# Kernel tuning notes

Measured on AMD Instinct MI355X. Metric: run time of the kernel, lower is better.

Reference implementation:

```python
import jax, jax.numpy as jnp
import numpy as np

B, N, DIM, HEADS = 2, 2048, 1152, 16
HD = DIM // HEADS  # 72


def _fake_quant_sym(x, axis):
    # Dynamic symmetric int8 fake-quant: per-row scale = max|x| / 127
    amax = jnp.max(jnp.abs(x), axis=axis, keepdims=True)
    scale = jnp.maximum(amax, 1e-8) / 127.0
    q = jnp.clip(jnp.round(x / scale), -128.0, 127.0) * scale
    return x + jax.lax.stop_gradient(q - x)  # STE


def _fake_quant_unsigned(x, axis):
    # Post-softmax attn map in [0,1]: unsigned 8-bit dynamic fake-quant
    amax = jnp.max(x, axis=axis, keepdims=True)
    scale = jnp.maximum(amax, 1e-8) / 255.0
    q = jnp.clip(jnp.round(x / scale), 0.0, 255.0) * scale
    return x + jax.lax.stop_gradient(q - x)


def setup_inputs() -> dict:
    key = jax.random.key(0)
    k1, k2, k3, k4 = jax.random.split(key, 4)
    return {
        "x": jax.random.normal(k1, (B, N, DIM), dtype=jnp.float32),
        "w_qkv": jax.random.normal(k2, (3 * DIM, DIM), dtype=jnp.float32) * 0.02,
        "w_proj": jax.random.normal(k3, (DIM, DIM), dtype=jnp.float32) * 0.02,
        "b_proj": jax.random.normal(k4, (DIM,), dtype=jnp.float32) * 0.02,
    }


def reference(x, w_qkv, w_proj, b_proj):
    Bsz, Nt, C = x.shape
    H, Dh = HEADS, C // HEADS
    qkv = x @ w_qkv.T  # [B, N, 3C]
    qkv = qkv.reshape(Bsz, Nt, 3, H, Dh).transpose(2, 0, 3, 1, 4)  # [3, B, H, N, Dh]
    q, k, v = qkv[0], qkv[1], qkv[2]
    # Dynamic quantization: q/k per (token) row over head_dim; v per channel over tokens
    q = _fake_quant_sym(q, axis=-1)
    k = _fake_quant_sym(k, axis=-1)
    v = _fake_quant_sym(v, axis=-2)
    scale = Dh ** -0.5
    attn = jnp.einsum('bhnd,bhmd->bhnm', q * scale, k).astype(jnp.float32)
    attn = jax.nn.softmax(attn, axis=-1).astype(x.dtype)
    attn = _fake_quant_unsigned(attn, axis=-1)
    out = jnp.einsum('bhnm,bhmd->bhnd', attn, v)  # [B, H, N, Dh]
    out = out.transpose(0, 2, 1, 3).reshape(Bsz, Nt, C)
    return out @ w_proj.T + b_proj
```

## Files before the change

kernel.cpp:

```cpp
#include <hip/hip_runtime.h>
#include <math.h>


typedef int   i32x4  __attribute__((ext_vector_type(4)));
typedef short bf16x8 __attribute__((ext_vector_type(8)));
typedef float f32x4  __attribute__((ext_vector_type(4)));

constexpr int Bz   = 2;
constexpr int Ntok = 2048;
constexpr int DIMC = 1152;
constexpr int H    = 16;
constexpr int HD_  = 72;
constexpr int Mrows = Bz * Ntok;
constexpr int C3    = 3 * DIMC;

__device__ __forceinline__ unsigned short f2bf(float f) {
  unsigned u = __float_as_uint(f);
  return (unsigned short)((u + 0x7fffu + ((u >> 16) & 1u)) >> 16);
}
__device__ __forceinline__ float bf2f(unsigned short h) {
  return __uint_as_float((unsigned)h << 16);
}
__device__ __forceinline__ void split1(float v, unsigned short& h,
                                       unsigned short& m, unsigned short& l) {
  h = f2bf(v); float r1 = v - bf2f(h);
  m = f2bf(r1); float r2 = r1 - bf2f(m);
  l = f2bf(r2);
}

__global__ __launch_bounds__(256)
void split3_kernel(const float* __restrict__ src, unsigned short* __restrict__ ph,
                   unsigned short* __restrict__ pm, unsigned short* __restrict__ pl,
                   int n4) {
  for (int i = blockIdx.x * 256 + threadIdx.x; i < n4; i += gridDim.x * 256) {
    float4 v = ((const float4*)src)[i];
    ushort4 h, m, l;
    split1(v.x, h.x, m.x, l.x);
    split1(v.y, h.y, m.y, l.y);
    split1(v.z, h.z, m.z, l.z);
    split1(v.w, h.w, m.w, l.w);
    ((ushort4*)ph)[i] = h;
    ((ushort4*)pm)[i] = m;
    ((ushort4*)pl)[i] = l;
  }
}

__device__ __forceinline__ void gload16(const void* g, void* l) {
  __builtin_amdgcn_global_load_lds(
      (const __attribute__((address_space(1))) unsigned int*)g,
      (__attribute__((address_space(3))) unsigned int*)l, 16, 0, 0);
}

template<bool BIAS>
__global__ __launch_bounds__(256)
void gemm3(const unsigned short* __restrict__ Ah, const unsigned short* __restrict__ Am,
           const unsigned short* __restrict__ Al,
           const unsigned short* __restrict__ Bh, const unsigned short* __restrict__ Bm,
           const unsigned short* __restrict__ Bl,
           const float* __restrict__ bias, float* __restrict__ C,
           int Md, int Nd, int Kd) {
  __shared__ __align__(16) unsigned short As[3][128 * 32];
  __shared__ __align__(16) unsigned short Bs[3][128 * 32];
  const int t = threadIdx.x, lane = t & 63, wv = t >> 6;
  const int r15 = lane & 15, h4 = lane >> 4;
  const int gx = gridDim.x;
  const int nwg = gx * gridDim.y;
  const int orig = blockIdx.y * gx + blockIdx.x;
  const int qq = nwg >> 3, rr = nwg & 7;
  const int xcd = orig & 7, loc = orig >> 3;
  const int wg = (xcd < rr) ? (xcd * (qq + 1) + loc)
                            : (rr * (qq + 1) + (xcd - rr) * qq + loc);
  const int bm = (wg / gx) << 7, bn = (wg % gx) << 7;
  const int wn = (wv & 1) << 6, wm = (wv >> 1) << 6;

  const unsigned short* Ap[3] = {Ah, Am, Al};
  const unsigned short* Bp[3] = {Bh, Bm, Bl};

  f32x4 acc[4][4];
#pragma unroll
  for (int i = 0; i < 4; ++i)
#pragma unroll
    for (int j = 0; j < 4; ++j) acc[i][j] = (f32x4){0.f, 0.f, 0.f, 0.f};

  const int lin0 = t * 16;
  const int r0 = lin0 >> 6, cb0 = lin0 & 63;
  const int lin1 = lin0 + 4096;
  const int r1 = lin1 >> 6, cb1 = lin1 & 63;

  for (int k0 = 0; k0 < Kd; k0 += 32) {
    __syncthreads();
#pragma unroll
    for (int p = 0; p < 3; ++p) {
      gload16((const char*)(Ap[p] + (size_t)(bm + r0) * Kd + k0) + cb0,
              (char*)&As[p][0] + lin0);
      gload16((const char*)(Ap[p] + (size_t)(bm + r1) * Kd + k0) + cb1,
              (char*)&As[p][0] + lin1);
      gload16((const char*)(Bp[p] + (size_t)(bn + r0) * Kd + k0) + cb0,
              (char*)&Bs[p][0] + lin0);
      gload16((const char*)(Bp[p] + (size_t)(bn + r1) * Kd + k0) + cb1,
              (char*)&Bs[p][0] + lin1);
    }
    __syncthreads();
    bf16x8 bf[3][4];
#pragma unroll
    for (int p = 0; p < 3; ++p)
#pragma unroll
      for (int c = 0; c < 4; ++c)
        bf[p][c] = *(const bf16x8*)&Bs[p][(wn + c * 16 + r15) * 32 + h4 * 8];
#pragma unroll
    for (int pa = 0; pa < 3; ++pa) {
#pragma unroll
      for (int mf = 0; mf < 4; ++mf) {
        bf16x8 af = *(const bf16x8*)&As[pa][(wm + mf * 16 + r15) * 32 + h4 * 8];
#pragma unroll
        for (int bp = 0; bp < 3; ++bp) {
          if (bp < 3 - pa) {
#pragma unroll
            for (int nf = 0; nf < 4; ++nf)
              acc[mf][nf] = __builtin_amdgcn_mfma_f32_16x16x32_bf16(
                  bf[bp][nf], af, acc[mf][nf], 0, 0, 0);
          }
        }
      }
    }
  }
#pragma unroll
  for (int mf = 0; mf < 4; ++mf) {
    const int m = bm + wm + mf * 16 + r15;
#pragma unroll
    for (int nf = 0; nf < 4; ++nf) {
      const int n = bn + wn + nf * 16 + (h4 << 2);
      float4 o;
      o.x = acc[mf][nf][0]; o.y = acc[mf][nf][1];
      o.z = acc[mf][nf][2]; o.w = acc[mf][nf][3];
      if (BIAS) {
        o.x += bias[n]; o.y += bias[n + 1]; o.z += bias[n + 2]; o.w += bias[n + 3];
      }
      *(float4*)(C + (size_t)m * Nd + n) = o;
    }
  }
}

template<bool BIAS>
__global__ __launch_bounds__(256)
void gemm_bt(const float* __restrict__ A, const float* __restrict__ W,
             const float* __restrict__ bias, float* __restrict__ Cout,
             int Md, int Nd, int Kd) {
  __shared__ float As[16][132];
  __shared__ float Bs[16][132];
  const int t  = threadIdx.x;
  const int bm = blockIdx.y << 7, bn = blockIdx.x << 7;
  const int lr = t >> 1;
  const int lk = (t & 1) << 3;
  const float* Ap = A + (size_t)(bm + lr) * Kd + lk;
  const float* Wp = W + (size_t)(bn + lr) * Kd + lk;
  const int tx = t & 15, ty = t >> 4;
  float acc[8][8] = {};
  for (int k0 = 0; k0 < Kd; k0 += 16) {
    float4 a0 = *(const float4*)(Ap + k0);
    float4 a1 = *(const float4*)(Ap + k0 + 4);
    float4 w0 = *(const float4*)(Wp + k0);
    float4 w1 = *(const float4*)(Wp + k0 + 4);
    __syncthreads();
    As[lk + 0][lr] = a0.x; As[lk + 1][lr] = a0.y;
    As[lk + 2][lr] = a0.z; As[lk + 3][lr] = a0.w;
    As[lk + 4][lr] = a1.x; As[lk + 5][lr] = a1.y;
    As[lk + 6][lr] = a1.z; As[lk + 7][lr] = a1.w;
    Bs[lk + 0][lr] = w0.x; Bs[lk + 1][lr] = w0.y;
    Bs[lk + 2][lr] = w0.z; Bs[lk + 3][lr] = w0.w;
    Bs[lk + 4][lr] = w1.x; Bs[lk + 5][lr] = w1.y;
    Bs[lk + 6][lr] = w1.z; Bs[lk + 7][lr] = w1.w;
    __syncthreads();
#pragma unroll
    for (int kk = 0; kk < 16; ++kk) {
      float4 x0 = *(const float4*)&As[kk][(ty << 3) + 0];
      float4 x1 = *(const float4*)&As[kk][(ty << 3) + 4];
      float4 y0 = *(const float4*)&Bs[kk][(tx << 3) + 0];
      float4 y1 = *(const float4*)&Bs[kk][(tx << 3) + 4];
      float ar[8] = {x0.x, x0.y, x0.z, x0.w, x1.x, x1.y, x1.z, x1.w};
      float br[8] = {y0.x, y0.y, y0.z, y0.w, y1.x, y1.y, y1.z, y1.w};
#pragma unroll
      for (int i = 0; i < 8; ++i)
#pragma unroll
        for (int j = 0; j < 8; ++j)
          acc[i][j] = fmaf(ar[i], br[j], acc[i][j]);
    }
  }
  float bias8[8] = {0.f, 0.f, 0.f, 0.f, 0.f, 0.f, 0.f, 0.f};
  if (BIAS) {
#pragma unroll
    for (int j = 0; j < 8; ++j) bias8[j] = bias[bn + (tx << 3) + j];
  }
#pragma unroll
  for (int i = 0; i < 8; ++i) {
    const int m = bm + (ty << 3) + i;
    float* cp = Cout + (size_t)m * Nd + bn + (tx << 3);
    float4 o0, o1;
    o0.x = acc[i][0] + bias8[0]; o0.y = acc[i][1] + bias8[1];
    o0.z = acc[i][2] + bias8[2]; o0.w = acc[i][3] + bias8[3];
    o1.x = acc[i][4] + bias8[4]; o1.y = acc[i][5] + bias8[5];
    o1.z = acc[i][6] + bias8[6]; o1.w = acc[i][7] + bias8[7];
    *(float4*)(cp + 0) = o0;
    *(float4*)(cp + 4) = o1;
  }
}

__global__ __launch_bounds__(256)
void quant_qk_pack(const float* __restrict__ qkv,
                   signed char* __restrict__ q8, signed char* __restrict__ k8,
                   float* __restrict__ sq, float* __restrict__ sk) {
  const int wid  = (blockIdx.x << 2) + (threadIdx.x >> 6);
  const int lane = threadIdx.x & 63;
  const int h  = wid & 15;
  const int g  = (wid >> 4) & 1;
  const int bn = wid >> 5;
  const float* row = qkv + (size_t)bn * C3 + g * DIMC + h * HD_;
  float x0 = row[lane];
  float x1 = (lane < 8) ? row[64 + lane] : 0.f;
  float amax = fmaxf(fabsf(x0), fabsf(x1));
#pragma unroll
  for (int s = 32; s; s >>= 1) amax = fmaxf(amax, __shfl_xor(amax, s));
  const float scale = fmaxf(amax, 1e-8f) / 127.f;
  int q0 = (int)fminf(fmaxf(rintf(x0 / scale), -128.f), 127.f);
  int q1 = (int)fminf(fmaxf(rintf(x1 / scale), -128.f), 127.f);
  const int b = bn >> 11, n = bn & 2047;
  signed char* dst = (g ? k8 : q8) + ((size_t)(b * H + h) * Ntok + n) * 128;
  dst[lane] = (signed char)q0;
  dst[64 + lane] = (lane < 8) ? (signed char)q1 : 0;
  if (lane == 0) (g ? sk : sq)[(size_t)(b * H + h) * Ntok + n] = scale;
}

__global__ __launch_bounds__(256)
void quant_v_pack(const float* __restrict__ qkv, signed char* __restrict__ vT8,
                  float* __restrict__ sv, int* __restrict__ cs) {
  const int col = blockIdx.x;
  const int d = col % 80;
  const int h = (col / 80) % H;
  const int b = col / (80 * H);
  const int idx = (b * H + h) * 80 + d;
  signed char* vrow = vT8 + (size_t)idx * 2048;
  const int t = threadIdx.x;
  if (d >= HD_) {
#pragma unroll
    for (int i = 0; i < 8; ++i) vrow[t + (i << 8)] = 0;
    if (t == 0) { sv[idx] = 0.f; cs[idx] = 0; }
    return;
  }
  const float* base = qkv + (size_t)b * Ntok * C3 + 2 * DIMC + h * HD_ + d;
  float vals[8];
  float amax = 0.f;
#pragma unroll
  for (int i = 0; i < 8; ++i) {
    float v = base[(size_t)(t + (i << 8)) * C3];
    vals[i] = v;
    amax = fmaxf(amax, fabsf(v));
  }
#pragma unroll
  for (int s = 32; s; s >>= 1) amax = fmaxf(amax, __shfl_xor(amax, s));
  __shared__ float red[4];
  if ((t & 63) == 0) red[t >> 6] = amax;
  __syncthreads();
  amax = fmaxf(fmaxf(red[0], red[1]), fmaxf(red[2], red[3]));
  const float scale = fmaxf(amax, 1e-8f) / 127.f;
  int isum = 0;
#pragma unroll
  for (int i = 0; i < 8; ++i) {
    int q = (int)fminf(fmaxf(rintf(vals[i] / scale), -128.f), 127.f);
    vrow[t + (i << 8)] = (signed char)q;
    isum += q;
  }
#pragma unroll
  for (int s = 32; s; s >>= 1) isum += __shfl_xor(isum, s);
  __shared__ int ired[4];
  if ((t & 63) == 0) ired[t >> 6] = isum;
  __syncthreads();
  if (t == 0) {
    cs[idx] = ired[0] + ired[1] + ired[2] + ired[3];
    sv[idx] = scale;
  }
}

__device__ __forceinline__ float logitv(float cl, float skj, int a) {
  return cl * skj * (float)a;
}

#define STAGE_K(KT)                                                          \
  {                                                                          \
    _Pragma("unroll")                                                        \
    for (int c_ = 0; c_ < 2; ++c_) {                                         \
      const int L_ = (t + (c_ << 8)) << 4;                                   \
      const int row_ = L_ >> 7;                                              \
      const int col_ = L_ & 127;                                             \
      gload16(kgbase + (size_t)(KT) * 8192 + row_ * 128 +                    \
                  (col_ ^ ((row_ & 7) << 4)),                                \
              Ks + L_);                                                      \
    }                                                                        \
  }
#define STAGE_SK(KT)                                                         \
  if (t < 16) {                                                              \
    gload16(skgbase + (KT) * 256 + (t << 4), (signed char*)Sks + (t << 4));  \
  }
#define STAGE_V(KT)                                                          \
  {                                                                          \
    const int L_ = t << 4;                                                   \
    const int row_ = L_ >> 6, col_ = L_ & 63;                                \
    gload16(vgbase + (size_t)row_ * 2048 + (KT) * 64 +                       \
                (col_ ^ ((row_ & 3) << 4)),                                  \
            Vs + L_);                                                        \
    if (t < 64) {                                                            \
      const int L2_ = (t + 256) << 4;                                        \
      const int row2_ = L2_ >> 6, col2_ = L2_ & 63;                          \
      gload16(vgbase + (size_t)row2_ * 2048 + (KT) * 64 +                    \
                  (col2_ ^ ((row2_ & 3) << 4)),                              \
              Vs + L2_);                                                     \
    }                                                                        \
  }

#define BODYA                                                                 \
  {                                                                           \
    _Pragma("unroll")                                                         \
    for (int g_ = 0; g_ < 4; ++g_) {                                          \
      const int krow_ = (g_ << 4) + i16;                                      \
      const int kx_ = (krow_ & 7) << 4;                                       \
      const i32x4 kf0_ = *(const i32x4*)&Ks[krow_ * 128 + ((h4 << 4) ^ kx_)]; \
      const i32x4 kf1_ = *(const i32x4*)&Ks[krow_ * 128 + ((64 | (h4 << 4)) ^ kx_)]; \
      i32x4 acc_ = {0, 0, 0, 0};                                              \
      acc_ = __builtin_amdgcn_mfma_i32_16x16x64_i8(kf0_, qf0, acc_, 0, 0, 0); \
      acc_ = __builtin_amdgcn_mfma_i32_16x16x64_i8(kf1_, qf1, acc_, 0, 0, 0); \
      const float4 skv_ = *(const float4*)&Sks[(g_ << 4) + (h4 << 2)];        \
      mr4[g_] = fmaxf(mr4[g_], logitv(cl, skv_.x, acc_[0]));                  \
      mr4[g_] = fmaxf(mr4[g_], logitv(cl, skv_.y, acc_[1]));                  \
      mr4[g_] = fmaxf(mr4[g_], logitv(cl, skv_.z, acc_[2]));                  \
      mr4[g_] = fmaxf(mr4[g_], logitv(cl, skv_.w, acc_[3]));                  \
    }                                                                         \
  }

#define BODYB                                                                 \
  {                                                                           \
    _Pragma("unroll")                                                         \
    for (int g_ = 0; g_ < 4; ++g_) {                                          \
      const int krow_ = (g_ << 4) + i16;                                      \
      const int kx_ = (krow_ & 7) << 4;                                       \
      const i32x4 kf0_ = *(const i32x4*)&Ks[krow_ * 128 + ((h4 << 4) ^ kx_)]; \
      const i32x4 kf1_ = *(const i32x4*)&Ks[krow_ * 128 + ((64 | (h4 << 4)) ^ kx_)]; \
      i32x4 acc_ = {0, 0, 0, 0};                                              \
      acc_ = __builtin_amdgcn_mfma_i32_16x16x64_i8(kf0_, qf0, acc_, 0, 0, 0); \
      acc_ = __builtin_amdgcn_mfma_i32_16x16x64_i8(kf1_, qf1, acc_, 0, 0, 0); \
      const float4 skv_ = *(const float4*)&Sks[(g_ << 4) + (h4 << 2)];        \
      const float sks_[4] = {skv_.x, skv_.y, skv_.z, skv_.w};                 \
      int packed_ = 0;                                                        \
      _Pragma("unroll")                                                       \
      for (int r_ = 0; r_ < 4; ++r_) {                                        \
        const float lv_ = logitv(cl, sks_[r_], acc_[r_]);                     \
        const float e_ = __expf(lv_ - mrow);            \
        z4[g_] += e_;                                                         \
        const float u_ = fminf(rintf(e_ * 255.f), 255.f);                     \
        const int s8_ = (int)u_ - 128;                                        \
        packed_ |= (s8_ & 255) << (r_ << 3);                                  \
      }                                                                       \
      *(int*)&P[wv][(i16 << 6) + ((g_ ^ sI) << 4) + (h4 << 2)] = packed_;     \
    }                                                                         \
    const i32x4 pf_ = *(const i32x4*)&P[wv][(i16 << 6) + ((h4 ^ sI) << 4)];   \
    _Pragma("unroll")                                                         \
    for (int dg_ = 0; dg_ < 5; ++dg_) {                                       \
      const int vrow_ = (dg_ << 4) + i16;                                     \
      const int vx_ = (vrow_ & 3) << 4;                                       \
      const i32x4 vf_ = *(const i32x4*)&Vs[vrow_ * 64 + ((h4 << 4) ^ vx_)];   \
      pv[dg_] = __builtin_amdgcn_mfma_i32_16x16x64_i8(vf_, pf_, pv[dg_], 0, 0, 0); \
    }                                                                         \
  }

template<bool SPLIT>
__global__ __launch_bounds__(256)
void attn_mfma(const signed char* __restrict__ q8, const signed char* __restrict__ k8,
               const signed char* __restrict__ vT8,
               const float* __restrict__ sq, const float* __restrict__ sk,
               const float* __restrict__ sv, const int* __restrict__ cs,
               float* __restrict__ aoutF,
               unsigned short* __restrict__ ah, unsigned short* __restrict__ am,
               unsigned short* __restrict__ al) {
  const int bid = ((blockIdx.x & 7) << 7) + (blockIdx.x >> 3);
  const int qt = bid & 31, h = (bid >> 5) & 15, b = bid >> 9;
  const int n0 = qt << 6;
  const int t = threadIdx.x, lane = t & 63, wv = t >> 6;
  const int i16 = lane & 15, h4 = lane >> 4;
  const int bh = b * H + h;
  const int sI = (i16 >> 1) & 3;

  __shared__ __align__(16) signed char Ks[8192];
  __shared__ __align__(16) signed char Vs[5120];
  __shared__ __align__(16) float Sks[64];
  __shared__ __align__(16) signed char P[4][1024];

  const int qrow = n0 + (wv << 4) + i16;
  const signed char* qp = q8 + ((size_t)bh * Ntok + qrow) * 128 + (h4 << 4);
  const i32x4 qf0 = *(const i32x4*)qp;
  const i32x4 qf1 = *(const i32x4*)(qp + 64);
  const float cl = sq[(size_t)bh * Ntok + qrow] * 0.11785113019775793f;
  const signed char* kgbase  = k8 + (size_t)bh * Ntok * 128;
  const signed char* vgbase  = vT8 + (size_t)bh * 80 * 2048;
  const signed char* skgbase = (const signed char*)(sk + (size_t)bh * Ntok);

  float mr4[4];
#pragma unroll
  for (int g = 0; g < 4; ++g) mr4[g] = -3.4e38f;
  for (int kt = 0; kt < 32; ++kt) {
    __syncthreads();
    STAGE_K(kt);
    STAGE_SK(kt);
    __syncthreads();
    BODYA;
  }
  float mrow = fmaxf(fmaxf(mr4[0], mr4[1]), fmaxf(mr4[2], mr4[3]));
  mrow = fmaxf(mrow, __shfl_xor(mrow, 16));
  mrow = fmaxf(mrow, __shfl_xor(mrow, 32));

  float z4[4] = {0.f, 0.f, 0.f, 0.f};
  i32x4 pv[5];
#pragma unroll
  for (int dg = 0; dg < 5; ++dg) pv[dg] = (i32x4){0, 0, 0, 0};

  for (int kt = 0; kt < 32; ++kt) {
    __syncthreads();
    STAGE_K(kt);
    STAGE_V(kt);
    STAGE_SK(kt);
    __syncthreads();
    BODYB;
  }

  float z = (z4[0] + z4[1]) + (z4[2] + z4[3]);
  z += __shfl_xor(z, 16);
  z += __shfl_xor(z, 32);
  const float rz = 1.0f / z;
  const float ss = rz / 255.f;

  const size_t rowoff = ((size_t)(b * Ntok + n0 + (wv << 4) + i16)) * DIMC + h * HD_;
  const int sbase = bh * 80;
#pragma unroll
  for (int dg = 0; dg < 5; ++dg) {
    const int d0 = dg * 16 + (h4 << 2);
    if (d0 < HD_) {
      float4 o;
      int t0 = pv[dg][0] + (cs[sbase + d0 + 0] << 7);
      int t1 = pv[dg][1] + (cs[sbase + d0 + 1] << 7);
      int t2 = pv[dg][2] + (cs[sbase + d0 + 2] << 7);
      int t3 = pv[dg][3] + (cs[sbase + d0 + 3] << 7);
      o.x = (float)t0 * sv[sbase + d0 + 0] * ss;
      o.y = (float)t1 * sv[sbase + d0 + 1] * ss;
      o.z = (float)t2 * sv[sbase + d0 + 2] * ss;
      o.w = (float)t3 * sv[sbase + d0 + 3] * ss;
      if (SPLIT) {
        ushort4 hh, mm, ll;
        split1(o.x, hh.x, mm.x, ll.x);
        split1(o.y, hh.y, mm.y, ll.y);
        split1(o.z, hh.z, mm.z, ll.z);
        split1(o.w, hh.w, mm.w, ll.w);
        *(ushort4*)(ah + rowoff + d0) = hh;
        *(ushort4*)(am + rowoff + d0) = mm;
        *(ushort4*)(al + rowoff + d0) = ll;
      } else {
        *(float4*)(aoutF + rowoff + d0) = o;
      }
    }
  }
}

constexpr size_t SZ_QKV  = (size_t)Mrows * C3 * 4;
constexpr size_t PL_X    = (size_t)Mrows * DIMC * 2;
constexpr size_t PL_WQ   = (size_t)C3 * DIMC * 2;
constexpr size_t PL_WP   = (size_t)DIMC * DIMC * 2;
constexpr size_t OFF_XA  = SZ_QKV;
constexpr size_t OFF_WQ  = OFF_XA + 3 * PL_X;
constexpr size_t OFF_WP  = OFF_WQ + 3 * PL_WQ;
constexpr size_t REQ_NEW = OFF_WP + 3 * PL_WP;
constexpr size_t SZ_Q8 = (size_t)Bz * H * Ntok * 128;
constexpr size_t SZ_V8 = (size_t)Bz * H * 80 * 2048;
constexpr size_t SZ_S  = (size_t)Bz * H * Ntok * 4;
constexpr size_t SZ_SV = (size_t)Bz * H * 80 * 4;
constexpr size_t A_Q8 = OFF_WQ;
constexpr size_t A_K8 = A_Q8 + SZ_Q8;
constexpr size_t A_V8 = A_K8 + SZ_Q8;
constexpr size_t A_SQ = A_V8 + SZ_V8;
constexpr size_t A_SK = A_SQ + SZ_S;
constexpr size_t A_SV = A_SK + SZ_S;
constexpr size_t A_CS = A_SV + SZ_SV;
static_assert(A_CS + SZ_SV <= OFF_WP, "alias overflow");
constexpr size_t F_AOUT = SZ_QKV;
constexpr size_t F_Q8   = F_AOUT + (size_t)Mrows * DIMC * 4;
constexpr size_t F_K8   = F_Q8 + SZ_Q8;
constexpr size_t F_V8   = F_K8 + SZ_Q8;
constexpr size_t F_SQ   = F_V8 + SZ_V8;
constexpr size_t F_SK   = F_SQ + SZ_S;
constexpr size_t F_SV   = F_SK + SZ_S;
constexpr size_t F_CS   = F_SV + SZ_SV;

extern "C" void kernel_launch(void* const* d_in, const int* in_sizes, int n_in,
                              void* d_out, int out_size, void* d_ws, size_t ws_size,
                              hipStream_t stream) {
  const float* x      = (const float*)d_in[0];
  const float* w_qkv  = (const float*)d_in[1];
  const float* w_proj = (const float*)d_in[2];
  const float* b_proj = (const float*)d_in[3];
  float* out = (float*)d_out;
  char* ws = (char*)d_ws;
  float* qkv = (float*)ws;

  if (ws_size >= REQ_NEW) {
    unsigned short* xh = (unsigned short*)(ws + OFF_XA);
    unsigned short* xm = xh + PL_X / 2;
    unsigned short* xl = xm + PL_X / 2;
    unsigned short* wqh = (unsigned short*)(ws + OFF_WQ);
    unsigned short* wqm = wqh + PL_WQ / 2;
    unsigned short* wql = wqm + PL_WQ / 2;
    unsigned short* wph = (unsigned short*)(ws + OFF_WP);
    unsigned short* wpm = wph + PL_WP / 2;
    unsigned short* wpl = wpm + PL_WP / 2;
    signed char* q8  = (signed char*)(ws + A_Q8);
    signed char* k8  = (signed char*)(ws + A_K8);
    signed char* vT8 = (signed char*)(ws + A_V8);
    float* sq = (float*)(ws + A_SQ);
    float* sk = (float*)(ws + A_SK);
    float* sv = (float*)(ws + A_SV);
    int*   cs = (int*)(ws + A_CS);
    unsigned short* ah = xh;
    unsigned short* am = xm;
    unsigned short* al = xl;

    split3_kernel<<<2048, 256, 0, stream>>>(x, xh, xm, xl, Mrows * DIMC / 4);
    split3_kernel<<<2048, 256, 0, stream>>>(w_qkv, wqh, wqm, wql, C3 * DIMC / 4);
    split3_kernel<<<1297, 256, 0, stream>>>(w_proj, wph, wpm, wpl, DIMC * DIMC / 4);
    gemm3<false><<<dim3(C3 / 128, Mrows / 128), 256, 0, stream>>>(
        xh, xm, xl, wqh, wqm, wql, nullptr, qkv, Mrows, C3, DIMC);
    quant_qk_pack<<<(Bz * Ntok * 2 * H) / 4, 256, 0, stream>>>(qkv, q8, k8, sq, sk);
    quant_v_pack<<<Bz * H * 80, 256, 0, stream>>>(qkv, vT8, sv, cs);
    attn_mfma<true><<<Bz * H * (Ntok / 64), 256, 0, stream>>>(
        q8, k8, vT8, sq, sk, sv, cs, nullptr, ah, am, al);
    gemm3<true><<<dim3(DIMC / 128, Mrows / 128), 256, 0, stream>>>(
        ah, am, al, wph, wpm, wpl, b_proj, out, Mrows, DIMC, DIMC);
  } else {
    float* aout = (float*)(ws + F_AOUT);
    signed char* q8  = (signed char*)(ws + F_Q8);
    signed char* k8  = (signed char*)(ws + F_K8);
    signed char* vT8 = (signed char*)(ws + F_V8);
    float* sq = (float*)(ws + F_SQ);
    float* sk = (float*)(ws + F_SK);
    float* sv = (float*)(ws + F_SV);
    int*   cs = (int*)(ws + F_CS);
    gemm_bt<false><<<dim3(C3 / 128, Mrows / 128), 256, 0, stream>>>(
        x, w_qkv, nullptr, qkv, Mrows, C3, DIMC);
    quant_qk_pack<<<(Bz * Ntok * 2 * H) / 4, 256, 0, stream>>>(qkv, q8, k8, sq, sk);
    quant_v_pack<<<Bz * H * 80, 256, 0, stream>>>(qkv, vT8, sv, cs);
    attn_mfma<false><<<Bz * H * (Ntok / 64), 256, 0, stream>>>(
        q8, k8, vT8, sq, sk, sv, cs, aout, nullptr, nullptr, nullptr);
    gemm_bt<true><<<dim3(DIMC / 128, Mrows / 128), 256, 0, stream>>>(
        aout, w_proj, b_proj, out, Mrows, DIMC, DIMC);
  }
}
```

Measured before the change: 504.1 us.

## Swizzle packed LDS layout in split-bf16 GEMM and narrow proj tile

```diff
diff --git a/kernel.cpp b/kernel.cpp
--- a/kernel.cpp
+++ b/kernel.cpp
@@ -51,7 +51,7 @@
       (__attribute__((address_space(3))) unsigned int*)l, 16, 0, 0);
 }
 
-template<bool BIAS>
+template<bool BIAS, int NF>
 __global__ __launch_bounds__(256)
 void gemm3(const unsigned short* __restrict__ Ah, const unsigned short* __restrict__ Am,
            const unsigned short* __restrict__ Al,
@@ -59,64 +59,88 @@
            const unsigned short* __restrict__ Bl,
            const float* __restrict__ bias, float* __restrict__ C,
            int Md, int Nd, int Kd) {
-  __shared__ __align__(16) unsigned short As[3][128 * 32];
-  __shared__ __align__(16) unsigned short Bs[3][128 * 32];
+  constexpr int BN = 32 * NF;
+  __shared__ __align__(16) char Apk[128 * 128];
+  __shared__ __align__(16) char Alt[128 * 64];
+  __shared__ __align__(16) char Bpk[BN * 128];
+  __shared__ __align__(16) char Blt[BN * 64];
   const int t = threadIdx.x, lane = t & 63, wv = t >> 6;
   const int r15 = lane & 15, h4 = lane >> 4;
   const int gx = gridDim.x;
   const int nwg = gx * gridDim.y;
   const int orig = blockIdx.y * gx + blockIdx.x;
-  const int qq = nwg >> 3, rr = nwg & 7;
-  const int xcd = orig & 7, loc = orig >> 3;
-  const int wg = (xcd < rr) ? (xcd * (qq + 1) + loc)
-                            : (rr * (qq + 1) + (xcd - rr) * qq + loc);
-  const int bm = (wg / gx) << 7, bn = (wg % gx) << 7;
-  const int wn = (wv & 1) << 6, wm = (wv >> 1) << 6;
-
-  const unsigned short* Ap[3] = {Ah, Am, Al};
-  const unsigned short* Bp[3] = {Bh, Bm, Bl};
-
-  f32x4 acc[4][4];
+  const int qq = nwg >> 3;
+  const int wg = (orig & 7) * qq + (orig >> 3);
+  const int bm = (wg / gx) << 7, bn = (wg % gx) * BN;
+  const int wn = (wv & 1) * (BN / 2), wm = (wv >> 1) << 6;
+
+  f32x4 acc[4][NF];
 #pragma unroll
   for (int i = 0; i < 4; ++i)
 #pragma unroll
-    for (int j = 0; j < 4; ++j) acc[i][j] = (f32x4){0.f, 0.f, 0.f, 0.f};
-
-  const int lin0 = t * 16;
-  const int r0 = lin0 >> 6, cb0 = lin0 & 63;
-  const int lin1 = lin0 + 4096;
-  const int r1 = lin1 >> 6, cb1 = lin1 & 63;
+    for (int j = 0; j < NF; ++j) acc[i][j] = (f32x4){0.f, 0.f, 0.f, 0.f};
+
+  const int k3 = (r15 & 7) << 4;
+  const int k2 = (r15 & 3) << 4;
 
   for (int k0 = 0; k0 < Kd; k0 += 32) {
     __syncthreads();
 #pragma unroll
-    for (int p = 0; p < 3; ++p) {
-      gload16((const char*)(Ap[p] + (size_t)(bm + r0) * Kd + k0) + cb0,
-              (char*)&As[p][0] + lin0);
-      gload16((const char*)(Ap[p] + (size_t)(bm + r1) * Kd + k0) + cb1,
-              (char*)&As[p][0] + lin1);
-      gload16((const char*)(Bp[p] + (size_t)(bn + r0) * Kd + k0) + cb0,
-              (char*)&Bs[p][0] + lin0);
-      gload16((const char*)(Bp[p] + (size_t)(bn + r1) * Kd + k0) + cb1,
-              (char*)&Bs[p][0] + lin1);
-    }
-    __syncthreads();
-    bf16x8 bf[3][4];
-#pragma unroll
-    for (int p = 0; p < 3; ++p)
-#pragma unroll
-      for (int c = 0; c < 4; ++c)
-        bf[p][c] = *(const bf16x8*)&Bs[p][(wn + c * 16 + r15) * 32 + h4 * 8];
+    for (int c = 0; c < 4; ++c) {
+      const int L = (t + (c << 8)) << 4;
+      const int row = L >> 7;
+      const int scol = (L & 127) ^ ((row & 7) << 4);
+      const unsigned short* sp = (scol & 64) ? Am : Ah;
+      gload16((const char*)(sp + (size_t)(bm + row) * Kd + k0) + (scol & 63),
+              Apk + L);
+    }
+#pragma unroll
+    for (int c = 0; c < 2; ++c) {
+      const int L = (t + (c << 8)) << 4;
+      const int row = L >> 6;
+      const int scol = (L & 63) ^ ((row & 3) << 4);
+      gload16((const char*)(Al + (size_t)(bm + row) * Kd + k0) + scol, Alt + L);
+    }
+#pragma unroll
+    for (int c = 0; c < NF; ++c) {
+      const int L = (t + (c << 8)) << 4;
+      const int row = L >> 7;
+      const int scol = (L & 127) ^ ((row & 7) << 4);
+      const unsigned short* sp = (scol & 64) ? Bm : Bh;
+      gload16((const char*)(sp + (size_t)(bn + row) * Kd + k0) + (scol & 63),
+              Bpk + L);
+    }
+#pragma unroll
+    for (int c = 0; c < NF / 2; ++c) {
+      const int L = (t + (c << 8)) << 4;
+      const int row = L >> 6;
+      const int scol = (L & 63) ^ ((row & 3) << 4);
+      gload16((const char*)(Bl + (size_t)(bn + row) * Kd + k0) + scol, Blt + L);
+    }
+    __syncthreads();
+
+    bf16x8 bf[3][NF];
+#pragma unroll
+    for (int c = 0; c < NF; ++c) {
+      const int br = wn + c * 16 + r15;
+      bf[0][c] = *(const bf16x8*)(Bpk + br * 128 + ((h4 << 4) ^ k3));
+      bf[1][c] = *(const bf16x8*)(Bpk + br * 128 + ((64 | (h4 << 4)) ^ k3));
+      bf[2][c] = *(const bf16x8*)(Blt + br * 64 + ((h4 << 4) ^ k2));
+    }
 #pragma unroll
     for (int pa = 0; pa < 3; ++pa) {
 #pragma unroll
       for (int mf = 0; mf < 4; ++mf) {
-        bf16x8 af = *(const bf16x8*)&As[pa][(wm + mf * 16 + r15) * 32 + h4 * 8];
+        const int ar = wm + mf * 16 + r15;
+        bf16x8 af;
+        if (pa == 0)      af = *(const bf16x8*)(Apk + ar * 128 + ((h4 << 4) ^ k3));
+        else if (pa == 1) af = *(const bf16x8*)(Apk + ar * 128 + ((64 | (h4 << 4)) ^ k3));
+        else              af = *(const bf16x8*)(Alt + ar * 64 + ((h4 << 4) ^ k2));
 #pragma unroll
         for (int bp = 0; bp < 3; ++bp) {
           if (bp < 3 - pa) {
 #pragma unroll
-            for (int nf = 0; nf < 4; ++nf)
+            for (int nf = 0; nf < NF; ++nf)
               acc[mf][nf] = __builtin_amdgcn_mfma_f32_16x16x32_bf16(
                   bf[bp][nf], af, acc[mf][nf], 0, 0, 0);
           }
@@ -128,7 +152,7 @@
   for (int mf = 0; mf < 4; ++mf) {
     const int m = bm + wm + mf * 16 + r15;
 #pragma unroll
-    for (int nf = 0; nf < 4; ++nf) {
+    for (int nf = 0; nf < NF; ++nf) {
       const int n = bn + wn + nf * 16 + (h4 << 2);
       float4 o;
       o.x = acc[mf][nf][0]; o.y = acc[mf][nf][1];
@@ -530,13 +554,13 @@
     split3_kernel<<<2048, 256, 0, stream>>>(x, xh, xm, xl, Mrows * DIMC / 4);
     split3_kernel<<<2048, 256, 0, stream>>>(w_qkv, wqh, wqm, wql, C3 * DIMC / 4);
     split3_kernel<<<1297, 256, 0, stream>>>(w_proj, wph, wpm, wpl, DIMC * DIMC / 4);
-    gemm3<false><<<dim3(C3 / 128, Mrows / 128), 256, 0, stream>>>(
+    gemm3<false, 4><<<dim3(C3 / 128, Mrows / 128), 256, 0, stream>>>(
         xh, xm, xl, wqh, wqm, wql, nullptr, qkv, Mrows, C3, DIMC);
     quant_qk_pack<<<(Bz * Ntok * 2 * H) / 4, 256, 0, stream>>>(qkv, q8, k8, sq, sk);
     quant_v_pack<<<Bz * H * 80, 256, 0, stream>>>(qkv, vT8, sv, cs);
     attn_mfma<true><<<Bz * H * (Ntok / 64), 256, 0, stream>>>(
         q8, k8, vT8, sq, sk, sv, cs, nullptr, ah, am, al);
-    gemm3<true><<<dim3(DIMC / 128, Mrows / 128), 256, 0, stream>>>(
+    gemm3<true, 2><<<dim3(DIMC / 64, Mrows / 128), 256, 0, stream>>>(
         ah, am, al, wph, wpm, wpl, b_proj, out, Mrows, DIMC, DIMC);
   } else {
     float* aout = (float*)(ws + F_AOUT);
```

New measurement: 496.0 us. About the same (-1.6%).
